# Performance work log

Measured on AMD Instinct MI355X. Metric: run time of the kernel, lower is better.

## Reference

```python
import jax, jax.numpy as jnp
import numpy as np

N_NODES = 50000
N_EDGES = 800000
IN_CH = 64
OUT_CH = 128
N_HEADS = 4
HEAD_DIM = OUT_CH // N_HEADS
LN_EPS = 1e-5


def setup_inputs() -> dict:
    key = jax.random.key(0)
    ks = jax.random.split(key, 12)
    def lin(k, fan_in, fan_out):
        bound = 1.0 / np.sqrt(fan_in)
        kw, kb = jax.random.split(k)
        W = jax.random.uniform(kw, (fan_in, fan_out), jnp.float32, -bound, bound)
        b = jax.random.uniform(kb, (fan_out,), jnp.float32, -bound, bound)
        return W, b
    Wq, bq = lin(ks[0], IN_CH, OUT_CH)
    Wk, bk = lin(ks[1], IN_CH, OUT_CH)
    Wv, bv = lin(ks[2], IN_CH, OUT_CH)
    We1, be1 = lin(ks[3], 2 * IN_CH, OUT_CH)
    We2, be2 = lin(ks[4], OUT_CH, N_HEADS)
    Wo, bo = lin(ks[5], OUT_CH, OUT_CH)
    gamma = jnp.ones((OUT_CH,), jnp.float32)
    beta = jnp.zeros((OUT_CH,), jnp.float32)
    x = jax.random.normal(ks[6], (N_NODES, IN_CH), jnp.float32)
    edge_index = jax.random.randint(ks[7], (2, N_EDGES), 0, N_NODES, jnp.int64 if jax.config.jax_enable_x64 else jnp.int32)
    return {"x": x, "edge_index": edge_index,
            "Wq": Wq, "bq": bq, "Wk": Wk, "bk": bk, "Wv": Wv, "bv": bv,
            "We1": We1, "be1": be1, "We2": We2, "be2": be2,
            "Wo": Wo, "bo": bo, "gamma": gamma, "beta": beta}


def reference(x, edge_index, Wq, bq, Wk, bk, Wv, bv, We1, be1, We2, be2, Wo, bo, gamma, beta):
    # Projections -> [N, H, Dh]
    q = (x @ Wq + bq).reshape(-1, N_HEADS, HEAD_DIM)
    k = (x @ Wk + bk).reshape(-1, N_HEADS, HEAD_DIM)
    v = (x @ Wv + bv).reshape(-1, N_HEADS, HEAD_DIM)
    src, dst = edge_index[0], edge_index[1]
    # Edge MLP attention weights: [E, H, 1]
    edge_features = jnp.concatenate([x[src], x[dst]], axis=-1)  # [E, 2*IN_CH]
    edge_weights = jax.nn.relu(edge_features @ We1 + be1) @ We2 + be2  # [E, H]
    edge_weights = edge_weights[:, :, None]
    # Attention logits per edge: [E, H, 1]
    attn = jnp.sum(q[dst] * k[src], axis=-1, keepdims=True)
    attn = attn * edge_weights / np.sqrt(HEAD_DIM).astype(np.float32)
    # Faithful to original: softmax over the edge dimension (dim=0)
    attn = jax.nn.softmax(attn, axis=0)
    # Weighted gather-scatter aggregation: [N, H, Dh]
    out = jax.ops.segment_sum(attn * v[src], dst, num_segments=N_NODES)
    out = out.reshape(-1, OUT_CH)
    # Output transform (dropout is identity in eval mode) + LayerNorm
    out = out @ Wo + bo
    mu = jnp.mean(out, axis=-1, keepdims=True)
    var = jnp.var(out, axis=-1, keepdims=True)
    out = (out - mu) * jax.lax.rsqrt(var + LN_EPS) * gamma + beta
    return out
```

## Files before the change

kernel.cpp:

```cpp
#include <hip/hip_runtime.h>
#include <hip/hip_bf16.h>

typedef __hip_bfloat16 bf16;
typedef __attribute__((ext_vector_type(8))) short short8;
typedef __attribute__((ext_vector_type(4))) float f32x4;
typedef __attribute__((ext_vector_type(2))) float f32x2;
typedef _Float16 h2 __attribute__((ext_vector_type(2)));

constexpr int NN = 50000;
constexpr int NE = 800000;
constexpr int IC = 64;
constexpr int OC = 128;
constexpr int NH = 4;
constexpr unsigned F32_ONE = 0x3F800000u;
constexpr float KC = 0.25503486f;

__device__ __forceinline__ float ldf(const void* p, int i, bool f32) {
    return f32 ? ((const float*)p)[i]
               : __bfloat162float(((const bf16*)p)[i]);
}

__device__ __forceinline__ int ld_idx(const void* p, long long i, bool i64) {
    return i64 ? (int)((const long long*)p)[i] : ((const int*)p)[i];
}

__device__ __forceinline__ bool probe_i64(const void* ei) {
    const unsigned* u = (const unsigned*)ei;
    return (u[1] | u[3] | u[5] | u[7]) == 0u;
}

__device__ __forceinline__ unsigned f2bu(float x) {
    unsigned u = __float_as_uint(x);
    return (u + 0x7FFFu + ((u >> 16) & 1u)) >> 16;
}

__device__ __forceinline__ h2 u2h(unsigned u) { return __builtin_bit_cast(h2, u); }

__device__ __forceinline__ float fdot2(h2 a, h2 b, float c) {
#if __has_builtin(__builtin_amdgcn_fdot2)
    return __builtin_amdgcn_fdot2(a, b, c, false);
#else
    return c + (float)a[0] * (float)b[0] + (float)a[1] * (float)b[1];
#endif
}

__device__ __forceinline__ h2 relu2(h2 a) {
    h2 z = {(_Float16)0.f, (_Float16)0.f};
#if __has_builtin(__builtin_elementwise_max)
    return __builtin_elementwise_max(a, z);
#else
    h2 r;
    r[0] = a[0] > (_Float16)0.f ? a[0] : (_Float16)0.f;
    r[1] = a[1] > (_Float16)0.f ? a[1] : (_Float16)0.f;
    return r;
#endif
}

#define DPPFADD(x, ctrl) \
    asm("v_add_f32 %0, %0, %0 " ctrl " row_mask:0xf bank_mask:0xf" : "+v"(x))

__device__ __forceinline__ int rfl(int v) { return __builtin_amdgcn_readfirstlane(v); }

__device__ __forceinline__ short8 ld_xrow(const void* x, bool f32, int m, int off) {
    if (!f32) return *(const short8*)((const bf16*)x + (size_t)m * IC + off);
    const float* xr = (const float*)x + (size_t)m * IC + off;
    float4 u0 = *(const float4*)xr;
    float4 u1 = *(const float4*)(xr + 4);
    short8 r;
    r[0] = (short)f2bu(u0.x); r[1] = (short)f2bu(u0.y);
    r[2] = (short)f2bu(u0.z); r[3] = (short)f2bu(u0.w);
    r[4] = (short)f2bu(u1.x); r[5] = (short)f2bu(u1.y);
    r[6] = (short)f2bu(u1.z); r[7] = (short)f2bu(u1.w);
    return r;
}

__device__ __forceinline__ unsigned char f32_to_fp8(float x) {
#if __has_builtin(__builtin_amdgcn_cvt_pk_fp8_f32)
    return (unsigned char)(__builtin_amdgcn_cvt_pk_fp8_f32(x, x, 0, false) & 0xFF);
#else
    unsigned bits = __float_as_uint(x);
    unsigned s = bits >> 31;
    float a = fabsf(x);
    if (a >= 448.f) return (unsigned char)((s << 7) | 0x7E);
    if (a < 0.015625f) {
        int m = (int)(a * 512.f + 0.5f);
        if (m >= 8) return (unsigned char)((s << 7) | 0x08);
        return (unsigned char)((s << 7) | m);
    }
    unsigned ab = (bits & 0x7FFFFFFFu) + 0x00080000u;
    int e8 = (int)(ab >> 23) - 127 + 7;
    unsigned m3 = (ab >> 20) & 7u;
    if (e8 >= 16) return (unsigned char)((s << 7) | 0x7E);
    return (unsigned char)((s << 7) | ((unsigned)e8 << 3) | m3);
#endif
}

__device__ __forceinline__ void fp8x2_to_f32(unsigned u, float& f0, float& f1) {
#if __has_builtin(__builtin_amdgcn_cvt_pk_f32_fp8)
    f32x2 lo = __builtin_amdgcn_cvt_pk_f32_fp8(u, false);
    f0 = lo[0]; f1 = lo[1];
#else
    float r[2];
#pragma unroll
    for (int j = 0; j < 2; ++j) {
        unsigned b = (u >> (8 * j)) & 0xFF;
        unsigned s = b >> 7, e = (b >> 3) & 15, m = b & 7;
        float v = (e == 0) ? (float)m * 0.001953125f
                           : __uint_as_float(((e + 120u) << 23) | (m << 20));
        r[j] = s ? -v : v;
    }
    f0 = r[0]; f1 = r[1];
#endif
}

constexpr int PB_W   = 160;
constexpr int PB_WO  = 64;
constexpr int PB_CNT = 3125;

__global__ __launch_bounds__(256) void prep(
    const void* __restrict__ Wq, const void* __restrict__ bq,
    const void* __restrict__ Wk, const void* __restrict__ bk,
    const void* __restrict__ Wv, const void* __restrict__ bv,
    const void* __restrict__ We1, const void* __restrict__ be1,
    const void* __restrict__ We2, const void* __restrict__ be2,
    const void* __restrict__ Wo,  const unsigned* __restrict__ gw,
    const void* __restrict__ eia, const void* __restrict__ eib, int split,
    bf16* __restrict__ WcatT, bf16* __restrict__ WoT,
    int* __restrict__ cnt, int* __restrict__ rank,
    unsigned* __restrict__ We2h, float* __restrict__ be2f,
    float* __restrict__ bcat)
{
    const bool f32 = (gw[0] == F32_ONE);
    int b = blockIdx.x, t = threadIdx.x;
    if (b < PB_W) {
        int idx = b * 256 + t;
        int n = idx >> 6, k = idx & 63;
        int sel = n >> 7, c = n & 127;
        float v;
        if (sel == 0)      v = ldf(Wq, k * OC + c, f32);
        else if (sel == 1) v = ldf(Wk, k * OC + c, f32);
        else if (sel == 2) v = ldf(Wv, k * OC + c, f32);
        else if (sel == 3) v = ldf(We1, k * OC + c, f32);
        else               v = ldf(We1, (IC + k) * OC + c, f32);
        WcatT[idx] = __float2bfloat16(v);
    } else if (b < PB_W + PB_WO) {
        int idx = (b - PB_W) * 256 + t;
        int n = idx >> 7, k = idx & 127;
        WoT[idx] = __float2bfloat16(ldf(Wo, k * OC + n, f32));
    } else if (b < PB_W + PB_WO + PB_CNT) {
        const bool i64 = probe_i64(eia);
        long long e = (long long)(b - PB_W - PB_WO) * 256 + t;
        int d = split ? ld_idx(eib, e, i64) : ld_idx(eia, NE + e, i64);
        int r = atomicAdd(&cnt[d], 1);
        rank[e] = r;
    } else {
        if (t < NH) be2f[t] = ldf(be2, t, f32);
        {
            int ln = t >> 2, k = t & 3;
            int g = ln >> 4, ii = ln & 15;
            int pp = 4 * ii + k;
            h2 hv;
            hv[0] = (_Float16)ldf(We2, (2 * pp) * NH + g, f32);
            hv[1] = (_Float16)ldf(We2, (2 * pp + 1) * NH + g, f32);
            We2h[t] = __builtin_bit_cast(unsigned, hv);
        }
        for (int n = t; n < 5 * OC; n += 256) {
            int sel = n >> 7, c = n & 127;
            float bb = 0.f;
            if (sel == 0) bb = ldf(bq, c, f32);
            else if (sel == 1) bb = ldf(bk, c, f32);
            else if (sel == 2) bb = ldf(bv, c, f32);
            else if (sel == 4) bb = ldf(be1, c, f32);
            bcat[n] = bb;
        }
    }
}

constexpr int SCAN_NB = 49;

__global__ __launch_bounds__(256) void scan_part(const int* __restrict__ cnt,
                                                 int* __restrict__ bsum,
                                                 int* __restrict__ rowptr)
{
    int b = blockIdx.x, t = threadIdx.x;
    int base = b * 1024 + t * 4;
    int4 v;
    if (base < NN) v = *(const int4*)(cnt + base);
    else { v.x = 0; v.y = 0; v.z = 0; v.w = 0; }
    int s = v.x + v.y + v.z + v.w;
#pragma unroll
    for (int off = 1; off < 64; off <<= 1) s += __shfl_xor(s, off);
    __shared__ int sm[4];
    int lane = t & 63, w = t >> 6;
    if (lane == 0) sm[w] = s;
    __syncthreads();
    if (t == 0) bsum[b] = sm[0] + sm[1] + sm[2] + sm[3];
    if (b == 0 && t == 0) rowptr[NN] = NE;
}

__global__ __launch_bounds__(256) void scan_fin(const int* __restrict__ cnt,
                                                const int* __restrict__ bsum,
                                                int* __restrict__ rowptr)
{
    int b = blockIdx.x, t = threadIdx.x;
    int lane = t & 63, w = t >> 6;
    __shared__ int s_boff;
    __shared__ int wsum[4];
    if (w == 0) {
        int pre = (lane < b) ? bsum[lane] : 0;
#pragma unroll
        for (int off = 1; off < 64; off <<= 1) pre += __shfl_xor(pre, off);
        if (lane == 0) s_boff = pre;
    }
    int base = b * 1024 + t * 4;
    int4 v;
    if (base < NN) v = *(const int4*)(cnt + base);
    else { v.x = 0; v.y = 0; v.z = 0; v.w = 0; }
    int s = v.x + v.y + v.z + v.w;
    int inc = s;
#pragma unroll
    for (int off = 1; off < 64; off <<= 1) {
        int u = __shfl_up(inc, off);
        if (lane >= off) inc += u;
    }
    if (lane == 63) wsum[w] = inc;
    __syncthreads();
    int run = s_boff + (inc - s);
#pragma unroll
    for (int i = 0; i < 3; ++i) if (i < w) run += wsum[i];
    if (base < NN) {
        int4 rp;
        rp.x = run;
        rp.y = rp.x + v.x;
        rp.z = rp.y + v.y;
        rp.w = rp.z + v.z;
        *(int4*)(rowptr + base) = rp;
    }
}

constexpr int NG_GEMM = 3125;
constexpr int NG_FILL = 3125;

__global__ __launch_bounds__(256) void node_gemm(
    const void* __restrict__ x, const unsigned* __restrict__ gw,
    const bf16* __restrict__ WcatT,
    const float* __restrict__ bcat,
    unsigned char* __restrict__ qb_dst, unsigned char* __restrict__ ka_src,
    unsigned char* __restrict__ vf8,
    const void* __restrict__ eia, const void* __restrict__ eib, int split,
    const int* __restrict__ rowptr, const int* __restrict__ rank,
    int* __restrict__ ssrc)
{
    __shared__ _Float16 qbs[16][264];
    __shared__ _Float16 kas[16][264];
    __shared__ unsigned char vfs[16][144];

    if (blockIdx.x >= NG_GEMM) {
        const bool i64 = probe_i64(eia);
        long long e = (long long)(blockIdx.x - NG_GEMM) * 256 + threadIdx.x;
        int s = ld_idx(eia, e, i64);
        int d = split ? ld_idx(eib, e, i64) : ld_idx(eia, NE + e, i64);
        int pos = rowptr[d] + rank[e];
        ssrc[pos] = s;
        return;
    }
    const bool f32 = (gw[0] == F32_ONE);
    int wave = threadIdx.x >> 6;
    int lane = threadIdx.x & 63;
    int quad = lane >> 4;
    int l16  = lane & 15;
    int row_base = blockIdx.x * 16;
    int m = row_base + l16;

    short8 a0 = ld_xrow(x, f32, m, quad * 8);
    short8 a1 = ld_xrow(x, f32, m, 32 + quad * 8);

#pragma unroll
    for (int t = 0; t < 10; ++t) {
        int colbase = wave * 160 + t * 16;
        const bf16* bp = WcatT + (size_t)(colbase + l16) * IC + quad * 8;
        short8 b0 = *(const short8*)(bp);
        short8 b1 = *(const short8*)(bp + 32);
        f32x4 acc = {0.f, 0.f, 0.f, 0.f};
        acc = __builtin_amdgcn_mfma_f32_16x16x32_bf16(a0, b0, acc, 0, 0, 0);
        acc = __builtin_amdgcn_mfma_f32_16x16x32_bf16(a1, b1, acc, 0, 0, 0);

        float bias = bcat[colbase + l16];
        int sel = colbase >> 7;
        int cc  = (colbase & 127) + l16;
#pragma unroll
        for (int r = 0; r < 4; ++r) {
            int l = quad * 4 + r;
            float fv = acc[r] + bias;
            if (sel == 2) {
                vfs[l][cc] = f32_to_fp8(fv);
            } else {
                _Float16 val = (_Float16)fv;
                if (sel == 0)      qbs[l][cc] = val;
                else if (sel == 1) kas[l][cc] = val;
                else if (sel == 3) kas[l][128 + cc] = val;
                else               qbs[l][128 + cc] = val;
            }
        }
    }
    __syncthreads();

    int tix = threadIdx.x;
#pragma unroll
    for (int j = 0; j < 2; ++j) {
        int i = tix + j * 256;
        int row = i >> 5, idx = i & 31;
        *(uint4*)(qb_dst + (size_t)(row_base + row) * 512 + idx * 16) =
            *(const uint4*)((const char*)&qbs[row][0] + idx * 16);
        *(uint4*)(ka_src + (size_t)(row_base + row) * 512 + idx * 16) =
            *(const uint4*)((const char*)&kas[row][0] + idx * 16);
    }
    if (tix < 128) {
        int row = tix >> 3, idx = tix & 7;
        *(uint4*)(vf8 + (size_t)(row_base + row) * OC + idx * 16) =
            *(const uint4*)((const char*)&vfs[row][0] + idx * 16);
    }
}

__global__ __launch_bounds__(256) void edge_gather(
    const int* __restrict__ rowptr, const int* __restrict__ ssrc,
    unsigned char* __restrict__ qb_dst, const unsigned char* __restrict__ ka_src,
    const unsigned char* __restrict__ vf8,
    const unsigned* __restrict__ We2h, const float* __restrict__ be2f,
    float* __restrict__ spart)
{
    int node = rfl(blockIdx.x * 4 + (threadIdx.x >> 6));
    int lane = threadIdx.x & 63;
    int i16  = lane & 15;
    int myh  = lane >> 4;

    const unsigned char* drow = qb_dst + (size_t)node * 512;
    h2 dq = u2h(*(const unsigned*)(drow + lane * 4));
    uint4 dbu = *(const uint4*)(drow + 256 + 16 * i16);
    h2 db0 = u2h(dbu.x), db1 = u2h(dbu.y), db2 = u2h(dbu.z), db3 = u2h(dbu.w);

    uint4 wu = *(const uint4*)(We2h + lane * 4);
    h2 w0 = u2h(wu.x), w1 = u2h(wu.y), w2 = u2h(wu.z), w3 = u2h(wu.w);
    float be2h = be2f[myh];

    int beg = rfl(rowptr[node]);
    int end = rfl(rowptr[node + 1]);
    float o0 = 0.f, o1 = 0.f, s_acc = 0.f;

    if (beg < end) {
        int ib = (beg + 1 < end) ? beg + 1 : end - 1;
        int sa = rfl(ssrc[beg]);
        int sb = rfl(ssrc[ib]);
        const unsigned char* ra = ka_src + (size_t)sa * 512;
        const unsigned char* rb = ka_src + (size_t)sb * 512;
        unsigned kuA = *(const unsigned*)(ra + lane * 4);
        uint4    auA = *(const uint4*)(ra + 256 + 16 * i16);
        unsigned uvA = *(const unsigned short*)(vf8 + (size_t)sa * OC + 2 * lane);
        unsigned kuB = *(const unsigned*)(rb + lane * 4);
        uint4    auB = *(const uint4*)(rb + 256 + 16 * i16);
        unsigned uvB = *(const unsigned short*)(vf8 + (size_t)sb * OC + 2 * lane);
        int na = (beg + 2 < end) ? beg + 2 : end - 1;
        int nb = (beg + 3 < end) ? beg + 3 : end - 1;
        int sna = rfl(ssrc[na]);
        int snb = rfl(ssrc[nb]);

        for (int p = beg; p < end; p += 2) {
            const unsigned char* rc = ka_src + (size_t)sna * 512;
            const unsigned char* rd = ka_src + (size_t)snb * 512;
            unsigned kuC = *(const unsigned*)(rc + lane * 4);
            uint4    auC = *(const uint4*)(rc + 256 + 16 * i16);
            unsigned uvC = *(const unsigned short*)(vf8 + (size_t)sna * OC + 2 * lane);
            unsigned kuD = *(const unsigned*)(rd + lane * 4);
            uint4    auD = *(const uint4*)(rd + 256 + 16 * i16);
            unsigned uvD = *(const unsigned short*)(vf8 + (size_t)snb * OC + 2 * lane);
            int fa = (p + 4 < end) ? p + 4 : end - 1;
            int fb = (p + 5 < end) ? p + 5 : end - 1;
            int s4a = rfl(ssrc[fa]);
            int s4b = rfl(ssrc[fb]);

            bool hasB = (p + 1 < end);

            float tA = fdot2(u2h(kuA), dq, 0.f);
            float tB = fdot2(u2h(kuB), dq, 0.f);
            h2 hA0 = relu2(u2h(auA.x) + db0);
            h2 hA1 = relu2(u2h(auA.y) + db1);
            h2 hA2 = relu2(u2h(auA.z) + db2);
            h2 hA3 = relu2(u2h(auA.w) + db3);
            h2 hB0 = relu2(u2h(auB.x) + db0);
            h2 hB1 = relu2(u2h(auB.y) + db1);
            h2 hB2 = relu2(u2h(auB.z) + db2);
            h2 hB3 = relu2(u2h(auB.w) + db3);
            float pA = fdot2(hA3, w3, fdot2(hA2, w2, fdot2(hA1, w1, fdot2(hA0, w0, 0.f))));
            float pB = fdot2(hB3, w3, fdot2(hB2, w2, fdot2(hB1, w1, fdot2(hB0, w0, 0.f))));

            DPPFADD(tA, "quad_perm:[1,0,3,2]");  DPPFADD(pA, "quad_perm:[1,0,3,2]");
            DPPFADD(tB, "quad_perm:[1,0,3,2]");  DPPFADD(pB, "quad_perm:[1,0,3,2]");
            DPPFADD(tA, "quad_perm:[2,3,0,1]");  DPPFADD(pA, "quad_perm:[2,3,0,1]");
            DPPFADD(tB, "quad_perm:[2,3,0,1]");  DPPFADD(pB, "quad_perm:[2,3,0,1]");
            DPPFADD(tA, "row_ror:8");            DPPFADD(pA, "row_ror:8");
            DPPFADD(tB, "row_ror:8");            DPPFADD(pB, "row_ror:8");
            DPPFADD(tA, "row_ror:4");            DPPFADD(pA, "row_ror:4");
            DPPFADD(tB, "row_ror:4");            DPPFADD(pB, "row_ror:4");

            float coefA = exp2f(tA * (pA + be2h) * KC);
            float coefB = hasB ? exp2f(tB * (pB + be2h) * KC) : 0.f;
            s_acc += coefA + coefB;

            float vA0, vA1, vB0, vB1;
            fp8x2_to_f32(uvA, vA0, vA1);
            fp8x2_to_f32(uvB, vB0, vB1);
            o0 = fmaf(coefA, vA0, fmaf(coefB, vB0, o0));
            o1 = fmaf(coefA, vA1, fmaf(coefB, vB1, o1));

            kuA = kuC; auA = auC; uvA = uvC;
            kuB = kuD; auB = auD; uvB = uvD;
            sna = s4a; snb = s4b;
        }
    }
    *(unsigned*)(qb_dst + (size_t)node * 512 + lane * 4) = f2bu(o0) | (f2bu(o1) << 16);
    if (i16 == 0) spart[node * 4 + myh] = s_acc;
}

constexpr int SR_BLOCKS = 98;
__global__ __launch_bounds__(256) void s_reduce(const float* __restrict__ spart,
                                                float* __restrict__ ssum)
{
    int tid = blockIdx.x * 256 + threadIdx.x;
    int h = threadIdx.x & 3;
    float s = 0.f;
    for (int i = tid; i < NN * 4; i += SR_BLOCKS * 256) s += spart[i];
#pragma unroll
    for (int off = 4; off <= 32; off <<= 1) s += __shfl_xor(s, off);
    __shared__ float sm[4][4];
    int lane = threadIdx.x & 63, w = threadIdx.x >> 6;
    if (lane < 4) sm[w][h] = s;
    __syncthreads();
    if (threadIdx.x < 4) {
        float tot = sm[0][h] + sm[1][h] + sm[2][h] + sm[3][h];
        atomicAdd(&ssum[h], tot);
    }
}

__global__ __launch_bounds__(256) void out_gemm(
    const unsigned char* __restrict__ aggv, const bf16* __restrict__ WoT,
    const void* __restrict__ bo, const void* __restrict__ gamma,
    const void* __restrict__ beta, const unsigned* __restrict__ gw,
    const float* __restrict__ ssum,
    void* __restrict__ out)
{
    const bool f32 = (gw[0] == F32_ONE);
    int wave = threadIdx.x >> 6;
    int lane = threadIdx.x & 63;
    int quad = lane >> 4;
    int l16  = lane & 15;
    int rb = blockIdx.x * 64 + wave * 16;
    int m = rb + l16;
    int ma = (m < NN) ? m : 0;

    const bf16* arow = (const bf16*)(aggv + (size_t)ma * 512);
    short8 a[4];
#pragma unroll
    for (int h = 0; h < 4; ++h) {
        short8 raw = *(const short8*)(arow + h * 32 + quad * 8);
        float invh = 1.0f / ssum[h];
#pragma unroll
        for (int jj = 0; jj < 8; ++jj) {
            float f = __uint_as_float(((unsigned)(unsigned short)raw[jj]) << 16) * invh;
            raw[jj] = (short)f2bu(f);
        }
        a[h] = raw;
    }

    float o[8][4];
#pragma unroll
    for (int t = 0; t < 8; ++t) {
        const bf16* bp = WoT + (size_t)(t * 16 + l16) * OC + quad * 8;
        f32x4 acc = {0.f, 0.f, 0.f, 0.f};
#pragma unroll
        for (int h = 0; h < 4; ++h) {
            short8 bfr = *(const short8*)(bp + h * 32);
            acc = __builtin_amdgcn_mfma_f32_16x16x32_bf16(a[h], bfr, acc, 0, 0, 0);
        }
        float bias = ldf(bo, t * 16 + l16, f32);
#pragma unroll
        for (int r = 0; r < 4; ++r) o[t][r] = acc[r] + bias;
    }

#pragma unroll
    for (int r = 0; r < 4; ++r) {
        float s1 = 0.f, s2 = 0.f;
#pragma unroll
        for (int t = 0; t < 8; ++t) { s1 += o[t][r]; s2 += o[t][r] * o[t][r]; }
#pragma unroll
        for (int off = 1; off <= 8; off <<= 1) {
            s1 += __shfl_xor(s1, off);
            s2 += __shfl_xor(s2, off);
        }
        float mu = s1 * (1.0f / OC);
        float var = fmaxf(s2 * (1.0f / OC) - mu * mu, 0.f);
        float rs = rsqrtf(var + 1e-5f);
        int node = rb + quad * 4 + r;
        if (node < NN) {
#pragma unroll
            for (int t = 0; t < 8; ++t) {
                int col = t * 16 + l16;
                float y = (o[t][r] - mu) * rs * ldf(gamma, col, f32) + ldf(beta, col, f32);
                if (f32) ((float*)out)[(size_t)node * OC + col] = y;
                else     ((bf16*)out)[(size_t)node * OC + col] = __float2bfloat16(y);
            }
        }
    }
}

extern "C" void kernel_launch(void* const* d_in, const int* in_sizes, int n_in,
                              void* d_out, int out_size, void* d_ws, size_t ws_size,
                              hipStream_t stream)
{
    int p = 0;
    const void* x   = d_in[p++];
    const void* eia = d_in[p++];
    const void* eib = eia;
    int split = 0;
    if (n_in >= 17) { eib = d_in[p++]; split = 1; }
    const void* Wq   = d_in[p++];
    const void* bq   = d_in[p++];
    const void* Wk   = d_in[p++];
    const void* bk   = d_in[p++];
    const void* Wv   = d_in[p++];
    const void* bv   = d_in[p++];
    const void* We1  = d_in[p++];
    const void* be1  = d_in[p++];
    const void* We2  = d_in[p++];
    const void* be2  = d_in[p++];
    const void* Wo   = d_in[p++];
    const void* bo   = d_in[p++];
    const void* gamma= d_in[p++];
    const void* beta = d_in[p++];
    const unsigned* gw = (const unsigned*)gamma;

    char* w = (char*)d_ws;
    unsigned char* qb_dst = (unsigned char*)w; w += (size_t)NN * 512;
    unsigned char* ka_src = (unsigned char*)w; w += (size_t)NN * 512;
    unsigned char* vf8    = (unsigned char*)w; w += (size_t)NN * OC;
    int*   ssrc   = (int*)w;                   w += (size_t)NE * 4;
    int*   rank   = (int*)w;                   w += (size_t)NE * 4;
    int*   cnt    = (int*)w;                   w += (size_t)NN * 4;
    float* ssum   = (float*)w;                 w += 8 * 4;
    int*   rowptr = (int*)w;                   w += (size_t)(NN + 4) * 4;
    int*   bsum   = (int*)w;                   w += 64 * 4;
    float* spart  = (float*)w;                 w += (size_t)NN * 4 * 4;
    unsigned* We2h = (unsigned*)w;             w += 256 * 4;
    float* be2f   = (float*)w;                 w += NH * 4;
    bf16*  WcatT  = (bf16*)w;                  w += (size_t)5 * OC * IC * 2;
    float* bcat   = (float*)w;                 w += 5 * OC * 4;
    bf16*  WoT    = (bf16*)w;                  w += (size_t)OC * OC * 2;

    if (ws_size < (size_t)((char*)w - (char*)d_ws)) return;

    hipMemsetAsync(cnt, 0, (size_t)NN * 4 + 32, stream);
    prep<<<PB_W + PB_WO + PB_CNT + 1, 256, 0, stream>>>(
        Wq, bq, Wk, bk, Wv, bv, We1, be1, We2, be2, Wo, gw,
        eia, eib, split,
        WcatT, WoT, cnt, rank, We2h, be2f, bcat);
    scan_part<<<SCAN_NB, 256, 0, stream>>>(cnt, bsum, rowptr);
    scan_fin<<<SCAN_NB, 256, 0, stream>>>(cnt, bsum, rowptr);
    node_gemm<<<NG_GEMM + NG_FILL, 256, 0, stream>>>(
        x, gw, WcatT, bcat, qb_dst, ka_src, vf8, eia, eib, split, rowptr, rank, ssrc);
    edge_gather<<<NN / 4, 256, 0, stream>>>(rowptr, ssrc, qb_dst, ka_src, vf8,
                                            We2h, be2f, spart);
    s_reduce<<<SR_BLOCKS, 256, 0, stream>>>(spart, ssum);
    out_gemm<<<(NN + 63) / 64, 256, 0, stream>>>(qb_dst, WoT, bo, gamma, beta, gw,
                                                 ssum, d_out);
}
```

Measured before the change: 286.9 us.

## Make edge_gather persistent with atomic work queue and fused softmax sum reduction

Turns edge_gather into a persistent kernel with a fixed block count, where each wave pulls node indices from a global atomic counter instead of getting one node per wave from the grid. Each wave keeps a running per-head softmax denominator, reduces it in shared memory and adds it to ssum with atomics. This removes the separate s_reduce kernel and the spart buffer round-trip, and balances uneven node degrees. The cost is one atomic per node on a single counter, which can contend, plus a few more bytes zeroed in the memset.

```diff
diff --git a/kernel.cpp b/kernel.cpp
--- a/kernel.cpp
+++ b/kernel.cpp
@@ -322,122 +322,121 @@
     }
 }
 
+constexpr int EG_BLOCKS = 2048;
+
 __global__ __launch_bounds__(256) void edge_gather(
     const int* __restrict__ rowptr, const int* __restrict__ ssrc,
     unsigned char* __restrict__ qb_dst, const unsigned char* __restrict__ ka_src,
     const unsigned char* __restrict__ vf8,
     const unsigned* __restrict__ We2h, const float* __restrict__ be2f,
-    float* __restrict__ spart)
-{
-    int node = rfl(blockIdx.x * 4 + (threadIdx.x >> 6));
+    int* __restrict__ workctr, float* __restrict__ ssum)
+{
     int lane = threadIdx.x & 63;
     int i16  = lane & 15;
     int myh  = lane >> 4;
 
-    const unsigned char* drow = qb_dst + (size_t)node * 512;
-    h2 dq = u2h(*(const unsigned*)(drow + lane * 4));
-    uint4 dbu = *(const uint4*)(drow + 256 + 16 * i16);
-    h2 db0 = u2h(dbu.x), db1 = u2h(dbu.y), db2 = u2h(dbu.z), db3 = u2h(dbu.w);
-
     uint4 wu = *(const uint4*)(We2h + lane * 4);
     h2 w0 = u2h(wu.x), w1 = u2h(wu.y), w2 = u2h(wu.z), w3 = u2h(wu.w);
     float be2h = be2f[myh];
-
-    int beg = rfl(rowptr[node]);
-    int end = rfl(rowptr[node + 1]);
-    float o0 = 0.f, o1 = 0.f, s_acc = 0.f;
-
-    if (beg < end) {
-        int ib = (beg + 1 < end) ? beg + 1 : end - 1;
-        int sa = rfl(ssrc[beg]);
-        int sb = rfl(ssrc[ib]);
-        const unsigned char* ra = ka_src + (size_t)sa * 512;
-        const unsigned char* rb = ka_src + (size_t)sb * 512;
-        unsigned kuA = *(const unsigned*)(ra + lane * 4);
-        uint4    auA = *(const uint4*)(ra + 256 + 16 * i16);
-        unsigned uvA = *(const unsigned short*)(vf8 + (size_t)sa * OC + 2 * lane);
-        unsigned kuB = *(const unsigned*)(rb + lane * 4);
-        uint4    auB = *(const uint4*)(rb + 256 + 16 * i16);
-        unsigned uvB = *(const unsigned short*)(vf8 + (size_t)sb * OC + 2 * lane);
-        int na = (beg + 2 < end) ? beg + 2 : end - 1;
-        int nb = (beg + 3 < end) ? beg + 3 : end - 1;
-        int sna = rfl(ssrc[na]);
-        int snb = rfl(ssrc[nb]);
-
-        for (int p = beg; p < end; p += 2) {
-            const unsigned char* rc = ka_src + (size_t)sna * 512;
-            const unsigned char* rd = ka_src + (size_t)snb * 512;
-            unsigned kuC = *(const unsigned*)(rc + lane * 4);
-            uint4    auC = *(const uint4*)(rc + 256 + 16 * i16);
-            unsigned uvC = *(const unsigned short*)(vf8 + (size_t)sna * OC + 2 * lane);
-            unsigned kuD = *(const unsigned*)(rd + lane * 4);
-            uint4    auD = *(const uint4*)(rd + 256 + 16 * i16);
-            unsigned uvD = *(const unsigned short*)(vf8 + (size_t)snb * OC + 2 * lane);
-            int fa = (p + 4 < end) ? p + 4 : end - 1;
-            int fb = (p + 5 < end) ? p + 5 : end - 1;
-            int s4a = rfl(ssrc[fa]);
-            int s4b = rfl(ssrc[fb]);
-
-            bool hasB = (p + 1 < end);
-
-            float tA = fdot2(u2h(kuA), dq, 0.f);
-            float tB = fdot2(u2h(kuB), dq, 0.f);
-            h2 hA0 = relu2(u2h(auA.x) + db0);
-            h2 hA1 = relu2(u2h(auA.y) + db1);
-            h2 hA2 = relu2(u2h(auA.z) + db2);
-            h2 hA3 = relu2(u2h(auA.w) + db3);
-            h2 hB0 = relu2(u2h(auB.x) + db0);
-            h2 hB1 = relu2(u2h(auB.y) + db1);
-            h2 hB2 = relu2(u2h(auB.z) + db2);
-            h2 hB3 = relu2(u2h(auB.w) + db3);
-            float pA = fdot2(hA3, w3, fdot2(hA2, w2, fdot2(hA1, w1, fdot2(hA0, w0, 0.f))));
-            float pB = fdot2(hB3, w3, fdot2(hB2, w2, fdot2(hB1, w1, fdot2(hB0, w0, 0.f))));
-
-            DPPFADD(tA, "quad_perm:[1,0,3,2]");  DPPFADD(pA, "quad_perm:[1,0,3,2]");
-            DPPFADD(tB, "quad_perm:[1,0,3,2]");  DPPFADD(pB, "quad_perm:[1,0,3,2]");
-            DPPFADD(tA, "quad_perm:[2,3,0,1]");  DPPFADD(pA, "quad_perm:[2,3,0,1]");
-            DPPFADD(tB, "quad_perm:[2,3,0,1]");  DPPFADD(pB, "quad_perm:[2,3,0,1]");
-            DPPFADD(tA, "row_ror:8");            DPPFADD(pA, "row_ror:8");
-            DPPFADD(tB, "row_ror:8");            DPPFADD(pB, "row_ror:8");
-            DPPFADD(tA, "row_ror:4");            DPPFADD(pA, "row_ror:4");
-            DPPFADD(tB, "row_ror:4");            DPPFADD(pB, "row_ror:4");
-
-            float coefA = exp2f(tA * (pA + be2h) * KC);
-            float coefB = hasB ? exp2f(tB * (pB + be2h) * KC) : 0.f;
-            s_acc += coefA + coefB;
-
-            float vA0, vA1, vB0, vB1;
-            fp8x2_to_f32(uvA, vA0, vA1);
-            fp8x2_to_f32(uvB, vB0, vB1);
-            o0 = fmaf(coefA, vA0, fmaf(coefB, vB0, o0));
-            o1 = fmaf(coefA, vA1, fmaf(coefB, vB1, o1));
-
-            kuA = kuC; auA = auC; uvA = uvC;
-            kuB = kuD; auB = auD; uvB = uvD;
-            sna = s4a; snb = s4b;
-        }
-    }
-    *(unsigned*)(qb_dst + (size_t)node * 512 + lane * 4) = f2bu(o0) | (f2bu(o1) << 16);
-    if (i16 == 0) spart[node * 4 + myh] = s_acc;
-}
-
-constexpr int SR_BLOCKS = 98;
-__global__ __launch_bounds__(256) void s_reduce(const float* __restrict__ spart,
-                                                float* __restrict__ ssum)
-{
-    int tid = blockIdx.x * 256 + threadIdx.x;
-    int h = threadIdx.x & 3;
-    float s = 0.f;
-    for (int i = tid; i < NN * 4; i += SR_BLOCKS * 256) s += spart[i];
-#pragma unroll
-    for (int off = 4; off <= 32; off <<= 1) s += __shfl_xor(s, off);
+    float s_tot = 0.f;
+
+    for (;;) {
+        int n0 = 0;
+        if (lane == 0) n0 = atomicAdd(workctr, 1);
+        int node = rfl(n0);
+        if (node >= NN) break;
+
+        const unsigned char* drow = qb_dst + (size_t)node * 512;
+        h2 dq = u2h(*(const unsigned*)(drow + lane * 4));
+        uint4 dbu = *(const uint4*)(drow + 256 + 16 * i16);
+        h2 db0 = u2h(dbu.x), db1 = u2h(dbu.y), db2 = u2h(dbu.z), db3 = u2h(dbu.w);
+
+        int beg = rfl(rowptr[node]);
+        int end = rfl(rowptr[node + 1]);
+        float o0 = 0.f, o1 = 0.f, s_acc = 0.f;
+
+        if (beg < end) {
+            int ib = (beg + 1 < end) ? beg + 1 : end - 1;
+            int sa = rfl(ssrc[beg]);
+            int sb = rfl(ssrc[ib]);
+            const unsigned char* ra = ka_src + (size_t)sa * 512;
+            const unsigned char* rb = ka_src + (size_t)sb * 512;
+            unsigned kuA = *(const unsigned*)(ra + lane * 4);
+            uint4    auA = *(const uint4*)(ra + 256 + 16 * i16);
+            unsigned uvA = *(const unsigned short*)(vf8 + (size_t)sa * OC + 2 * lane);
+            unsigned kuB = *(const unsigned*)(rb + lane * 4);
+            uint4    auB = *(const uint4*)(rb + 256 + 16 * i16);
+            unsigned uvB = *(const unsigned short*)(vf8 + (size_t)sb * OC + 2 * lane);
+            int na = (beg + 2 < end) ? beg + 2 : end - 1;
+            int nb = (beg + 3 < end) ? beg + 3 : end - 1;
+            int sna = rfl(ssrc[na]);
+            int snb = rfl(ssrc[nb]);
+
+            for (int p = beg; p < end; p += 2) {
+                const unsigned char* rc = ka_src + (size_t)sna * 512;
+                const unsigned char* rd = ka_src + (size_t)snb * 512;
+                unsigned kuC = *(const unsigned*)(rc + lane * 4);
+                uint4    auC = *(const uint4*)(rc + 256 + 16 * i16);
+                unsigned uvC = *(const unsigned short*)(vf8 + (size_t)sna * OC + 2 * lane);
+                unsigned kuD = *(const unsigned*)(rd + lane * 4);
+                uint4    auD = *(const uint4*)(rd + 256 + 16 * i16);
+                unsigned uvD = *(const unsigned short*)(vf8 + (size_t)snb * OC + 2 * lane);
+                int fa = (p + 4 < end) ? p + 4 : end - 1;
+                int fb = (p + 5 < end) ? p + 5 : end - 1;
+                int s4a = rfl(ssrc[fa]);
+                int s4b = rfl(ssrc[fb]);
+
+                bool hasB = (p + 1 < end);
+
+                float tA = fdot2(u2h(kuA), dq, 0.f);
+                float tB = fdot2(u2h(kuB), dq, 0.f);
+                h2 hA0 = relu2(u2h(auA.x) + db0);
+                h2 hA1 = relu2(u2h(auA.y) + db1);
+                h2 hA2 = relu2(u2h(auA.z) + db2);
+                h2 hA3 = relu2(u2h(auA.w) + db3);
+                h2 hB0 = relu2(u2h(auB.x) + db0);
+                h2 hB1 = relu2(u2h(auB.y) + db1);
+                h2 hB2 = relu2(u2h(auB.z) + db2);
+                h2 hB3 = relu2(u2h(auB.w) + db3);
+                float pA = fdot2(hA3, w3, fdot2(hA2, w2, fdot2(hA1, w1, fdot2(hA0, w0, 0.f))));
+                float pB = fdot2(hB3, w3, fdot2(hB2, w2, fdot2(hB1, w1, fdot2(hB0, w0, 0.f))));
+
+                DPPFADD(tA, "quad_perm:[1,0,3,2]");  DPPFADD(pA, "quad_perm:[1,0,3,2]");
+                DPPFADD(tB, "quad_perm:[1,0,3,2]");  DPPFADD(pB, "quad_perm:[1,0,3,2]");
+                DPPFADD(tA, "quad_perm:[2,3,0,1]");  DPPFADD(pA, "quad_perm:[2,3,0,1]");
+                DPPFADD(tB, "quad_perm:[2,3,0,1]");  DPPFADD(pB, "quad_perm:[2,3,0,1]");
+                DPPFADD(tA, "row_ror:8");            DPPFADD(pA, "row_ror:8");
+                DPPFADD(tB, "row_ror:8");            DPPFADD(pB, "row_ror:8");
+                DPPFADD(tA, "row_ror:4");            DPPFADD(pA, "row_ror:4");
+                DPPFADD(tB, "row_ror:4");            DPPFADD(pB, "row_ror:4");
+
+                float coefA = exp2f(tA * (pA + be2h) * KC);
+                float coefB = hasB ? exp2f(tB * (pB + be2h) * KC) : 0.f;
+                s_acc += coefA + coefB;
+
+                float vA0, vA1, vB0, vB1;
+                fp8x2_to_f32(uvA, vA0, vA1);
+                fp8x2_to_f32(uvB, vB0, vB1);
+                o0 = fmaf(coefA, vA0, fmaf(coefB, vB0, o0));
+                o1 = fmaf(coefA, vA1, fmaf(coefB, vB1, o1));
+
+                kuA = kuC; auA = auC; uvA = uvC;
+                kuB = kuD; auB = auD; uvB = uvD;
+                sna = s4a; snb = s4b;
+            }
+        }
+        *(unsigned*)(qb_dst + (size_t)node * 512 + lane * 4) = f2bu(o0) | (f2bu(o1) << 16);
+        s_tot += s_acc;
+    }
+
     __shared__ float sm[4][4];
-    int lane = threadIdx.x & 63, w = threadIdx.x >> 6;
-    if (lane < 4) sm[w][h] = s;
+    int w = threadIdx.x >> 6;
+    if (i16 == 0) sm[w][myh] = s_tot;
     __syncthreads();
     if (threadIdx.x < 4) {
-        float tot = sm[0][h] + sm[1][h] + sm[2][h] + sm[3][h];
-        atomicAdd(&ssum[h], tot);
+        float tot = sm[0][threadIdx.x] + sm[1][threadIdx.x] +
+                    sm[2][threadIdx.x] + sm[3][threadIdx.x];
+        atomicAdd(&ssum[threadIdx.x], tot);
     }
 }
 
@@ -546,9 +545,9 @@
     int*   rank   = (int*)w;                   w += (size_t)NE * 4;
     int*   cnt    = (int*)w;                   w += (size_t)NN * 4;
     float* ssum   = (float*)w;                 w += 8 * 4;
+    int*   workctr= (int*)w;                   w += 4 * 4;
     int*   rowptr = (int*)w;                   w += (size_t)(NN + 4) * 4;
     int*   bsum   = (int*)w;                   w += 64 * 4;
-    float* spart  = (float*)w;                 w += (size_t)NN * 4 * 4;
     unsigned* We2h = (unsigned*)w;             w += 256 * 4;
     float* be2f   = (float*)w;                 w += NH * 4;
     bf16*  WcatT  = (bf16*)w;                  w += (size_t)5 * OC * IC * 2;
@@ -557,7 +556,7 @@
 
     if (ws_size < (size_t)((char*)w - (char*)d_ws)) return;
 
-    hipMemsetAsync(cnt, 0, (size_t)NN * 4 + 32, stream);
+    hipMemsetAsync(cnt, 0, (size_t)NN * 4 + 48, stream);
     prep<<<PB_W + PB_WO + PB_CNT + 1, 256, 0, stream>>>(
         Wq, bq, Wk, bk, Wv, bv, We1, be1, We2, be2, Wo, gw,
         eia, eib, split,
@@ -566,9 +565,8 @@
     scan_fin<<<SCAN_NB, 256, 0, stream>>>(cnt, bsum, rowptr);
     node_gemm<<<NG_GEMM + NG_FILL, 256, 0, stream>>>(
         x, gw, WcatT, bcat, qb_dst, ka_src, vf8, eia, eib, split, rowptr, rank, ssrc);
-    edge_gather<<<NN / 4, 256, 0, stream>>>(rowptr, ssrc, qb_dst, ka_src, vf8,
-                                            We2h, be2f, spart);
-    s_reduce<<<SR_BLOCKS, 256, 0, stream>>>(spart, ssum);
+    edge_gather<<<EG_BLOCKS, 256, 0, stream>>>(rowptr, ssrc, qb_dst, ka_src, vf8,
+                                               We2h, be2f, workctr, ssum);
     out_gemm<<<(NN + 63) / 64, 256, 0, stream>>>(qb_dst, WoT, bo, gamma, beta, gw,
                                                  ssum, d_out);
 }
```

New measurement: 919.2 us. +220.4%, slower.
